# Optimization experiments

Hardware: AMD Instinct MI355X
Metric: run time of the kernel (lower is better)

Reference implementation:

```python
import jax, jax.numpy as jnp
import numpy as np

D_MODEL = 1024
NUM_HEADS = 16
HEAD_DIM = D_MODEL // NUM_HEADS


def setup_inputs() -> dict:
    key = jax.random.key(0)
    k0, k1, k2, k3, k4 = jax.random.split(key, 5)
    B, S, D = 4, 2048, D_MODEL
    std = np.sqrt(2.0 / (D + D)).astype(np.float32)
    return {
        "in_features": jax.random.normal(k0, (B, S, D), dtype=jnp.float32),
        "Wq": jax.random.normal(k1, (D, D), dtype=jnp.float32) * std,
        "Wk": jax.random.normal(k2, (D, D), dtype=jnp.float32) * std,
        "Wv": jax.random.normal(k3, (D, D), dtype=jnp.float32) * std,
        "Wo": jax.random.normal(k4, (D, D), dtype=jnp.float32) * std,
    }


def reference(in_features, Wq, Wk, Wv, Wo):
    B, S, D = in_features.shape
    H, Hd = NUM_HEADS, HEAD_DIM

    def split_heads(x):  # (B,S,D) -> (B,H,S,Hd)
        return x.reshape(B, S, H, Hd).transpose(0, 2, 1, 3)

    q = split_heads(in_features @ Wq.T)
    k = split_heads(in_features @ Wk.T)
    v = split_heads(in_features @ Wv.T)

    scale = 1.0 / jnp.sqrt(jnp.asarray(Hd, dtype=q.dtype))
    scores = jnp.einsum("bhsd,bhtd->bhst", q, k) * scale  # (B,H,S,S)
    causal = jnp.tril(jnp.ones((S, S), dtype=bool))  # (S,S)
    scores = jnp.where(causal[None, None], scores, -jnp.inf)
    attn = jax.nn.softmax(scores, axis=-1)
    out = jnp.einsum("bhst,bhtd->bhsd", attn, v)  # (B,H,S,Hd)
    out = out.transpose(0, 2, 1, 3).reshape(B, S, D)
    return out @ Wo.T
```

## Files before the change

### kernel.cpp

```cpp
#include <hip/hip_runtime.h>


typedef float f32x4 __attribute__((ext_vector_type(4)));
typedef short s16x8 __attribute__((ext_vector_type(8)));

#if __has_builtin(__builtin_amdgcn_exp2f)
#define EXP2(x) __builtin_amdgcn_exp2f(x)
#else
#define EXP2(x) exp2f(x)
#endif

__device__ __forceinline__ unsigned short f2bf(float f) {
  unsigned int u = __float_as_uint(f);
  u += 0x7fffu + ((u >> 16) & 1u);
  return (unsigned short)(u >> 16);
}

__device__ __forceinline__ unsigned int pk2bf(float f0, float f1) {
  return __builtin_amdgcn_perm(__float_as_uint(f1) + 0x8000u,
                               __float_as_uint(f0) + 0x8000u, 0x07060302u);
}

__device__ __forceinline__ unsigned int pk2bf_t(float f0, float f1) {
  return __builtin_amdgcn_perm(__float_as_uint(f1), __float_as_uint(f0), 0x07060302u);
}

__device__ __forceinline__ void gl_lds16(const short* g, short* lds) {
  __builtin_amdgcn_global_load_lds(
      (const __attribute__((address_space(1))) unsigned int*)g,
      (__attribute__((address_space(3))) unsigned int*)lds, 16, 0, 0);
}

__global__ __launch_bounds__(256) void cvt_kernel(const float4* __restrict__ s,
                                                  ushort4* __restrict__ d, int n4) {
  int i = blockIdx.x * blockDim.x + threadIdx.x;
  int stride = gridDim.x * blockDim.x;
  for (int idx = i; idx < n4; idx += stride) {
    float4 f = s[idx];
    ushort4 r;
    r.x = f2bf(f.x); r.y = f2bf(f.y); r.z = f2bf(f.z); r.w = f2bf(f.w);
    d[idx] = r;
  }
}

__global__ __launch_bounds__(256) void cvtw_kernel(const float4* __restrict__ w0,
                                                   const float4* __restrict__ w1,
                                                   const float4* __restrict__ w2,
                                                   const float4* __restrict__ w3,
                                                   ushort4* __restrict__ d0,
                                                   ushort4* __restrict__ d1,
                                                   ushort4* __restrict__ d2,
                                                   ushort4* __restrict__ d3) {
  const int n4 = 1024 * 1024 / 4;
  const float4* s;
  ushort4* d;
  switch (blockIdx.y) {
    case 0: s = w0; d = d0; break;
    case 1: s = w1; d = d1; break;
    case 2: s = w2; d = d2; break;
    default: s = w3; d = d3; break;
  }
  int i = blockIdx.x * blockDim.x + threadIdx.x;
  int stride = gridDim.x * blockDim.x;
  for (int idx = i; idx < n4; idx += stride) {
    float4 f = s[idx];
    ushort4 r;
    r.x = f2bf(f.x); r.y = f2bf(f.y); r.z = f2bf(f.z); r.w = f2bf(f.w);
    d[idx] = r;
  }
}

template <int MODE>
__global__ __launch_bounds__(256) void gemm_bt(const short* __restrict__ A,
                                               const short* __restrict__ B,
                                               float* __restrict__ Cf,
                                               short* __restrict__ q_o,
                                               short* __restrict__ k_o,
                                               short* __restrict__ vT_o,
                                               int M, int N, int K) {
  const int tid = threadIdx.x;
  const int wave = tid >> 6, lane = tid & 63;
  const int quad = lane >> 4, l15 = lane & 15;
  const int m0 = blockIdx.x * 128, n0 = blockIdx.y * 128;
  const int wm = (wave >> 1) * 64, wn = (wave & 1) * 64;

  __shared__ __align__(16) short As[128 * 64];
  __shared__ __align__(16) short Bs[128 * 64];

  const f32x4 z4 = {0.f, 0.f, 0.f, 0.f};
  f32x4 acc[4][4];
  for (int i = 0; i < 4; ++i)
    for (int j = 0; j < 4; ++j) acc[i][j] = z4;

  for (int k0 = 0; k0 < K; k0 += 64) {
    __syncthreads();
    for (int i = 0; i < 4; ++i) {
      int c = wave * 4 + i;
      int r = c * 8 + (lane >> 3);
      int c8 = (lane & 7) ^ (r & 7);
      gl_lds16(A + (size_t)(m0 + r) * K + k0 + c8 * 8, As + c * 512 + lane * 8);
      gl_lds16(B + (size_t)(n0 + r) * K + k0 + c8 * 8, Bs + c * 512 + lane * 8);
    }
    __syncthreads();
    for (int kk = 0; kk < 64; kk += 32) {
      int c8b = (kk >> 3) + quad;
      s16x8 af[4], bfr[4];
      for (int mt = 0; mt < 4; ++mt) {
        int row = wm + mt * 16 + l15;
        af[mt] = *(const s16x8*)(As + row * 64 + ((c8b ^ (row & 7)) << 3));
      }
      for (int nt = 0; nt < 4; ++nt) {
        int row = wn + nt * 16 + l15;
        bfr[nt] = *(const s16x8*)(Bs + row * 64 + ((c8b ^ (row & 7)) << 3));
      }
      for (int mt = 0; mt < 4; ++mt)
        for (int nt = 0; nt < 4; ++nt)
          acc[mt][nt] = __builtin_amdgcn_mfma_f32_16x16x32_bf16(af[mt], bfr[nt],
                                                                acc[mt][nt], 0, 0, 0);
    }
  }

  if (MODE == 0) {
    for (int mt = 0; mt < 4; ++mt)
      for (int nt = 0; nt < 4; ++nt) {
        int col = n0 + wn + nt * 16 + l15;
        for (int r = 0; r < 4; ++r) {
          int row = m0 + wm + mt * 16 + quad * 4 + r;
          Cf[(size_t)row * N + col] = acc[mt][nt][r];
        }
      }
  } else {
    if (n0 < 1024) {
      const float scale = 0.18033688011112042f;
      for (int mt = 0; mt < 4; ++mt)
        for (int nt = 0; nt < 4; ++nt) {
          int col = n0 + wn + nt * 16 + l15;
          for (int r = 0; r < 4; ++r) {
            int row = m0 + wm + mt * 16 + quad * 4 + r;
            ((unsigned short*)q_o)[(size_t)row * 1024 + col] = f2bf(acc[mt][nt][r] * scale);
          }
        }
    } else if (n0 < 2048) {
      for (int mt = 0; mt < 4; ++mt)
        for (int nt = 0; nt < 4; ++nt) {
          int col = n0 - 1024 + wn + nt * 16 + l15;
          for (int r = 0; r < 4; ++r) {
            int row = m0 + wm + mt * 16 + quad * 4 + r;
            ((unsigned short*)k_o)[(size_t)row * 1024 + col] = f2bf(acc[mt][nt][r]);
          }
        }
    } else {
      for (int mt = 0; mt < 4; ++mt)
        for (int nt = 0; nt < 4; ++nt) {
          int col = n0 - 2048 + wn + nt * 16 + l15;
          int h = col >> 6, d = col & 63;
          int row0 = m0 + wm + mt * 16 + quad * 4;
          int b = row0 >> 11, s = row0 & 2047;
          uint2 pk;
          pk.x = pk2bf(acc[mt][nt][0], acc[mt][nt][1]);
          pk.y = pk2bf(acc[mt][nt][2], acc[mt][nt][3]);
          *(uint2*)((unsigned short*)vT_o + (((size_t)b * 16 + h) * 64 + d) * 2048 + s) = pk;
        }
    }
  }
}

__global__ __launch_bounds__(256, 3) void attn_kernel(const short* __restrict__ qb,
                                                      const short* __restrict__ kb,
                                                      const short* __restrict__ vT,
                                                      short* __restrict__ ob) {
  const int bh = blockIdx.x;
  const int qt = 15 - (int)blockIdx.y;
  const int tid = threadIdx.x;
  const int wave = tid >> 6, lane = tid & 63;
  const int quad = lane >> 4, l15 = lane & 15;
  const int q0 = qt * 128;
  const size_t rowbase = (size_t)(bh >> 4) * 2048;
  const int hoff = (bh & 15) * 64;

  __shared__ __align__(16) short Ks[8192];
  __shared__ __align__(16) short VTs[8192];
  __shared__ __align__(16) short Ps[10240];
  short* Pw = Ps + wave * 2560;

  s16x8 qf[2][2];
#pragma unroll
  for (int n = 0; n < 2; ++n) {
    const short* qrow = qb + (rowbase + q0 + wave * 32 + n * 16 + l15) * 1024 + hoff;
#pragma unroll
    for (int k2 = 0; k2 < 2; ++k2)
      qf[n][k2] = *(const s16x8*)(qrow + k2 * 32 + quad * 8);
  }

  const f32x4 z4 = {0.f, 0.f, 0.f, 0.f};
  f32x4 oacc[2][4];
#pragma unroll
  for (int n = 0; n < 2; ++n)
#pragma unroll
    for (int dt = 0; dt < 4; ++dt) oacc[n][dt] = z4;
  float lacc[2] = {0.f, 0.f};

  for (int t = 0; t <= qt; ++t) {
    __syncthreads();
#pragma unroll
    for (int i = 0; i < 4; ++i) {
      int c = wave * 4 + i;
      int r = c * 8 + (lane >> 3);
      int c8 = (lane & 7) ^ (r & 7);
      gl_lds16(kb + (rowbase + t * 128 + r) * 1024 + hoff + c8 * 8, Ks + c * 512 + lane * 8);
    }
#pragma unroll
    for (int i = 0; i < 4; ++i) {
      int c = wave * 4 + i;
      int d = c * 4 + (lane >> 4);
      int c8 = (lane & 15) ^ (d & 7);
      gl_lds16(vT + ((size_t)bh * 64 + d) * 2048 + t * 128 + c8 * 8, VTs + c * 512 + lane * 8);
    }
    __syncthreads();

    f32x4 sacc[2][8];
#pragma unroll
    for (int n = 0; n < 2; ++n)
#pragma unroll
      for (int m = 0; m < 8; ++m) sacc[n][m] = z4;
#pragma unroll
    for (int k2 = 0; k2 < 2; ++k2) {
#pragma unroll
      for (int m = 0; m < 8; ++m) {
        int row = m * 16 + l15;
        s16x8 kf = *(const s16x8*)(Ks + row * 64 + ((((k2 << 2) + quad) ^ (row & 7)) << 3));
        sacc[0][m] = __builtin_amdgcn_mfma_f32_16x16x32_bf16(kf, qf[0][k2], sacc[0][m], 0, 0, 0);
        sacc[1][m] = __builtin_amdgcn_mfma_f32_16x16x32_bf16(kf, qf[1][k2], sacc[1][m], 0, 0, 0);
      }
    }

    if (t == qt) {
#pragma unroll
      for (int n = 0; n < 2; ++n) {
        int qg = wave * 32 + n * 16 + l15;
#pragma unroll
        for (int m = 0; m < 8; ++m) {
          int kvb = m * 16 + quad * 4;
#pragma unroll
          for (int r = 0; r < 4; ++r)
            if (kvb + r > qg) sacc[n][m][r] = -1e30f;
        }
      }
    }

    uint2 pp[2][8];
#pragma unroll
    for (int n = 0; n < 2; ++n) {
      float sum = 0.f;
#pragma unroll
      for (int m = 0; m < 8; ++m) {
        float p0 = EXP2(sacc[n][m][0]);
        float p1 = EXP2(sacc[n][m][1]);
        float p2 = EXP2(sacc[n][m][2]);
        float p3 = EXP2(sacc[n][m][3]);
        sum += (p0 + p1) + (p2 + p3);
        pp[n][m].x = pk2bf_t(p0, p1);
        pp[n][m].y = pk2bf_t(p2, p3);
      }
      lacc[n] += sum;
    }

#pragma unroll
    for (int kk = 0; kk < 4; ++kk) {
      short* Pb = Pw + (kk & 1) * 1280;
#pragma unroll
      for (int n = 0; n < 2; ++n)
#pragma unroll
        for (int mm = 0; mm < 2; ++mm)
          *(uint2*)(Pb + (n * 16 + l15) * 40 + mm * 16 + quad * 4) = pp[n][2 * kk + mm];
      s16x8 pf0 = *(const s16x8*)(Pb + l15 * 40 + quad * 8);
      s16x8 pf1 = *(const s16x8*)(Pb + (16 + l15) * 40 + quad * 8);
#pragma unroll
      for (int dt = 0; dt < 4; ++dt) {
        int d = dt * 16 + l15;
        s16x8 vf = *(const s16x8*)(VTs + d * 128 + ((((kk << 2) + quad) ^ (d & 7)) << 3));
        oacc[0][dt] = __builtin_amdgcn_mfma_f32_16x16x32_bf16(vf, pf0, oacc[0][dt], 0, 0, 0);
        oacc[1][dt] = __builtin_amdgcn_mfma_f32_16x16x32_bf16(vf, pf1, oacc[1][dt], 0, 0, 0);
      }
    }
  }

#pragma unroll
  for (int n = 0; n < 2; ++n) {
    float l = lacc[n];
    l += __shfl_xor(l, 16);
    l += __shfl_xor(l, 32);
    float inv = 1.0f / l;
    size_t row = rowbase + q0 + wave * 32 + n * 16 + l15;
    unsigned short* orow = (unsigned short*)ob + row * 1024 + hoff;
#pragma unroll
    for (int dt = 0; dt < 4; ++dt) {
      f32x4 v = oacc[n][dt];
      uint2 pk;
      pk.x = pk2bf(v[0] * inv, v[1] * inv);
      pk.y = pk2bf(v[2] * inv, v[3] * inv);
      *(uint2*)(orow + dt * 16 + quad * 4) = pk;
    }
  }
}

extern "C" void kernel_launch(void* const* d_in, const int* in_sizes, int n_in,
                              void* d_out, int out_size, void* d_ws, size_t ws_size,
                              hipStream_t stream) {
  const float* X  = (const float*)d_in[0];
  const float* Wq = (const float*)d_in[1];
  const float* Wk = (const float*)d_in[2];
  const float* Wv = (const float*)d_in[3];
  const float* Wo = (const float*)d_in[4];

  short* xb   = (short*)d_ws;
  short* wqkv = xb + (size_t)8192 * 1024;
  short* wob  = wqkv + (size_t)3072 * 1024;
  short* qb   = wob + (size_t)1024 * 1024;
  short* kb   = qb + (size_t)8192 * 1024;
  short* vT   = kb + (size_t)8192 * 1024;
  short* ob   = xb;

  const int MB = 8192;

  cvt_kernel<<<2048, 256, 0, stream>>>((const float4*)X, (ushort4*)xb, MB * 1024 / 4);
  cvtw_kernel<<<dim3(128, 4), 256, 0, stream>>>(
      (const float4*)Wq, (const float4*)Wk, (const float4*)Wv, (const float4*)Wo,
      (ushort4*)wqkv, (ushort4*)(wqkv + 1024 * 1024), (ushort4*)(wqkv + 2 * 1024 * 1024),
      (ushort4*)wob);

  gemm_bt<1><<<dim3(64, 24), 256, 0, stream>>>(xb, wqkv, nullptr, qb, kb, vT, MB, 3072, 1024);

  attn_kernel<<<dim3(64, 16), 256, 0, stream>>>(qb, kb, vT, ob);

  gemm_bt<0><<<dim3(64, 8), 256, 0, stream>>>(ob, wob, (float*)d_out, nullptr, nullptr,
                                              nullptr, MB, 1024, 1024);
}
```

Baseline: 279.6 us.

## Double-buffer K tiles, load V directly to registers, merge conversion kernels

The attention kernel now double-buffers the K tile in LDS, prefetching tile t+1 while computing on tile t. This removes the second barrier per iteration. V^T fragments are read straight from global memory into registers, with the next 32-wide slice prefetched during the PV loop, so V no longer goes through LDS. The two fp32-to-bf16 conversion kernels are merged into one launch. In exchange, each wave issues uncoalesced-ish 16-byte global loads for V, which raises register pressure and global traffic, since V is now loaded per wave rather than shared through LDS.

Result: slower. 294.6 us (+5.4%).

```diff
diff --git a/kernel.cpp b/kernel.cpp
--- a/kernel.cpp
+++ b/kernel.cpp
@@ -31,42 +31,40 @@
       (__attribute__((address_space(3))) unsigned int*)lds, 16, 0, 0);
 }
 
-__global__ __launch_bounds__(256) void cvt_kernel(const float4* __restrict__ s,
-                                                  ushort4* __restrict__ d, int n4) {
+__global__ __launch_bounds__(256) void cvt_all(const float4* __restrict__ X,
+                                               const float4* __restrict__ Wq,
+                                               const float4* __restrict__ Wk,
+                                               const float4* __restrict__ Wv,
+                                               const float4* __restrict__ Wo,
+                                               ushort4* __restrict__ xb,
+                                               ushort4* __restrict__ wqkv,
+                                               ushort4* __restrict__ wob) {
+  const int NX = 8192 * 1024 / 4;
+  const int NW = 1024 * 1024 / 4;
+  const int NT = NX + 4 * NW;
   int i = blockIdx.x * blockDim.x + threadIdx.x;
   int stride = gridDim.x * blockDim.x;
-  for (int idx = i; idx < n4; idx += stride) {
-    float4 f = s[idx];
+  for (int idx = i; idx < NT; idx += stride) {
+    const float4* s;
+    ushort4* d;
+    int off;
+    if (idx < NX) {
+      s = X; d = xb; off = idx;
+    } else {
+      int j = idx - NX;
+      int w = j >> 18;
+      off = j & (NW - 1);
+      switch (w) {
+        case 0: s = Wq; d = wqkv; break;
+        case 1: s = Wk; d = wqkv + NW; break;
+        case 2: s = Wv; d = wqkv + 2 * NW; break;
+        default: s = Wo; d = wob; break;
+      }
+    }
+    float4 f = s[off];
     ushort4 r;
     r.x = f2bf(f.x); r.y = f2bf(f.y); r.z = f2bf(f.z); r.w = f2bf(f.w);
-    d[idx] = r;
-  }
-}
-
-__global__ __launch_bounds__(256) void cvtw_kernel(const float4* __restrict__ w0,
-                                                   const float4* __restrict__ w1,
-                                                   const float4* __restrict__ w2,
-                                                   const float4* __restrict__ w3,
-                                                   ushort4* __restrict__ d0,
-                                                   ushort4* __restrict__ d1,
-                                                   ushort4* __restrict__ d2,
-                                                   ushort4* __restrict__ d3) {
-  const int n4 = 1024 * 1024 / 4;
-  const float4* s;
-  ushort4* d;
-  switch (blockIdx.y) {
-    case 0: s = w0; d = d0; break;
-    case 1: s = w1; d = d1; break;
-    case 2: s = w2; d = d2; break;
-    default: s = w3; d = d3; break;
-  }
-  int i = blockIdx.x * blockDim.x + threadIdx.x;
-  int stride = gridDim.x * blockDim.x;
-  for (int idx = i; idx < n4; idx += stride) {
-    float4 f = s[idx];
-    ushort4 r;
-    r.x = f2bf(f.x); r.y = f2bf(f.y); r.z = f2bf(f.z); r.w = f2bf(f.w);
-    d[idx] = r;
+    d[off] = r;
   }
 }
 
@@ -178,11 +176,14 @@
   const size_t rowbase = (size_t)(bh >> 4) * 2048;
   const int hoff = (bh & 15) * 64;
 
-  __shared__ __align__(16) short Ks[8192];
-  __shared__ __align__(16) short VTs[8192];
+  __shared__ __align__(16) short Ks[2][8192];
   __shared__ __align__(16) short Ps[10240];
   short* Pw = Ps + wave * 2560;
 
+  const int sc = wave * 4;
+  const int sr0 = sc * 8 + (lane >> 3);
+  const int sc8 = (lane & 7);
+
   s16x8 qf[2][2];
 #pragma unroll
   for (int n = 0; n < 2; ++n) {
@@ -192,6 +193,13 @@
       qf[n][k2] = *(const s16x8*)(qrow + k2 * 32 + quad * 8);
   }
 
+#pragma unroll
+  for (int i = 0; i < 4; ++i) {
+    int r = sr0 + i * 8;
+    int c8 = sc8 ^ (r & 7);
+    gl_lds16(kb + (rowbase + r) * 1024 + hoff + c8 * 8, Ks[0] + (sc + i) * 512 + lane * 8);
+  }
+
   const f32x4 z4 = {0.f, 0.f, 0.f, 0.f};
   f32x4 oacc[2][4];
 #pragma unroll
@@ -200,23 +208,28 @@
     for (int dt = 0; dt < 4; ++dt) oacc[n][dt] = z4;
   float lacc[2] = {0.f, 0.f};
 
+  const short* vbase = vT + ((size_t)bh * 64 + l15) * 2048 + quad * 8;
+
   for (int t = 0; t <= qt; ++t) {
     __syncthreads();
-#pragma unroll
-    for (int i = 0; i < 4; ++i) {
-      int c = wave * 4 + i;
-      int r = c * 8 + (lane >> 3);
-      int c8 = (lane & 7) ^ (r & 7);
-      gl_lds16(kb + (rowbase + t * 128 + r) * 1024 + hoff + c8 * 8, Ks + c * 512 + lane * 8);
-    }
-#pragma unroll
-    for (int i = 0; i < 4; ++i) {
-      int c = wave * 4 + i;
-      int d = c * 4 + (lane >> 4);
-      int c8 = (lane & 15) ^ (d & 7);
-      gl_lds16(vT + ((size_t)bh * 64 + d) * 2048 + t * 128 + c8 * 8, VTs + c * 512 + lane * 8);
-    }
-    __syncthreads();
+
+    const short* vt = vbase + t * 128;
+    s16x8 vf0[4], vf1[4];
+#pragma unroll
+    for (int dt = 0; dt < 4; ++dt) vf0[dt] = *(const s16x8*)(vt + dt * 16 * 2048);
+
+    if (t < qt) {
+      short* kn = Ks[(t + 1) & 1];
+#pragma unroll
+      for (int i = 0; i < 4; ++i) {
+        int r = sr0 + i * 8;
+        int c8 = sc8 ^ (r & 7);
+        gl_lds16(kb + (rowbase + (t + 1) * 128 + r) * 1024 + hoff + c8 * 8,
+                 kn + (sc + i) * 512 + lane * 8);
+      }
+    }
+
+    const short* Kc = Ks[t & 1];
 
     f32x4 sacc[2][8];
 #pragma unroll
@@ -228,7 +241,7 @@
 #pragma unroll
       for (int m = 0; m < 8; ++m) {
         int row = m * 16 + l15;
-        s16x8 kf = *(const s16x8*)(Ks + row * 64 + ((((k2 << 2) + quad) ^ (row & 7)) << 3));
+        s16x8 kf = *(const s16x8*)(Kc + row * 64 + ((((k2 << 2) + quad) ^ (row & 7)) << 3));
         sacc[0][m] = __builtin_amdgcn_mfma_f32_16x16x32_bf16(kf, qf[0][k2], sacc[0][m], 0, 0, 0);
         sacc[1][m] = __builtin_amdgcn_mfma_f32_16x16x32_bf16(kf, qf[1][k2], sacc[1][m], 0, 0, 0);
       }
@@ -267,6 +280,13 @@
 
 #pragma unroll
     for (int kk = 0; kk < 4; ++kk) {
+      s16x8* vc = (kk & 1) ? vf1 : vf0;
+      if (kk < 3) {
+        s16x8* vn = (kk & 1) ? vf0 : vf1;
+#pragma unroll
+        for (int dt = 0; dt < 4; ++dt)
+          vn[dt] = *(const s16x8*)(vt + dt * 16 * 2048 + (kk + 1) * 32);
+      }
       short* Pb = Pw + (kk & 1) * 1280;
 #pragma unroll
       for (int n = 0; n < 2; ++n)
@@ -277,10 +297,8 @@
       s16x8 pf1 = *(const s16x8*)(Pb + (16 + l15) * 40 + quad * 8);
 #pragma unroll
       for (int dt = 0; dt < 4; ++dt) {
-        int d = dt * 16 + l15;
-        s16x8 vf = *(const s16x8*)(VTs + d * 128 + ((((kk << 2) + quad) ^ (d & 7)) << 3));
-        oacc[0][dt] = __builtin_amdgcn_mfma_f32_16x16x32_bf16(vf, pf0, oacc[0][dt], 0, 0, 0);
-        oacc[1][dt] = __builtin_amdgcn_mfma_f32_16x16x32_bf16(vf, pf1, oacc[1][dt], 0, 0, 0);
+        oacc[0][dt] = __builtin_amdgcn_mfma_f32_16x16x32_bf16(vc[dt], pf0, oacc[0][dt], 0, 0, 0);
+        oacc[1][dt] = __builtin_amdgcn_mfma_f32_16x16x32_bf16(vc[dt], pf1, oacc[1][dt], 0, 0, 0);
       }
     }
   }
@@ -323,11 +341,9 @@
 
   const int MB = 8192;
 
-  cvt_kernel<<<2048, 256, 0, stream>>>((const float4*)X, (ushort4*)xb, MB * 1024 / 4);
-  cvtw_kernel<<<dim3(128, 4), 256, 0, stream>>>(
-      (const float4*)Wq, (const float4*)Wk, (const float4*)Wv, (const float4*)Wo,
-      (ushort4*)wqkv, (ushort4*)(wqkv + 1024 * 1024), (ushort4*)(wqkv + 2 * 1024 * 1024),
-      (ushort4*)wob);
+  cvt_all<<<3072, 256, 0, stream>>>((const float4*)X, (const float4*)Wq, (const float4*)Wk,
+                                    (const float4*)Wv, (const float4*)Wo, (ushort4*)xb,
+                                    (ushort4*)wqkv, (ushort4*)wob);
 
   gemm_bt<1><<<dim3(64, 24), 256, 0, stream>>>(xb, wqkv, nullptr, qb, kb, vT, MB, 3072, 1024);
 
```
